# Optimization experiments

Hardware: AMD Instinct MI355X
Metric: run time of the kernel (lower is better)

## Reference

```python
import jax, jax.numpy as jnp
import numpy as np

B, F, H = 128, 12288, 2048   # batch, flattened-image dim (3x64x64), MLP hidden
TAU = 0.1                    # constraint(x) = relu(x@W1)@w2 - TAU  (so constraint(0) = -TAU < 0)
THRESHOLD = 1e-3
MAX_STEPS = 30


def setup_inputs() -> dict:
    key = jax.random.key(0)
    k1, k2, k3 = jax.random.split(key, 3)
    x0 = jnp.zeros((B, F), jnp.float32)                 # anchor point, constraint(x0) < 0 by construction
    x = jax.random.normal(k1, (B, F), jnp.float32)
    W1 = jax.random.normal(k2, (F, H), jnp.float32) / np.float32(np.sqrt(F))
    w2 = jax.random.normal(k3, (H,), jnp.float32) / np.float32(np.sqrt(H))
    return {"x0": x0, "x": x, "W1": W1, "w2": w2}


def reference(x0, x, W1, w2):
    def fvals(c):  # per-sample constraint value at interpolation coeff c: [B]
        xc = (1.0 - c)[:, None] * x0 + c[:, None] * x
        return jax.nn.relu(xc @ W1) @ w2 - TAU

    # f(0) = -TAU < 0 (asserted in original). Check f(1): samples already feasible skip search.
    f1 = fvals(jnp.ones((B,), jnp.float32))
    inside = f1 <= 0.0

    a = jnp.zeros((B,), jnp.float32)
    b = jnp.ones((B,), jnp.float32)
    c = jnp.ones((B,), jnp.float32)
    done = inside  # feasible samples keep c = 1 (projected == x)

    def step(carry, _):
        a, b, c, done = carry
        cm = (a + b) * 0.5
        v = fvals(cm)
        upd = ~done
        hit = upd & (v >= -THRESHOLD) & (v < 0.0)   # -threshold <= f(c) < 0 -> converged
        go_a = upd & (v < 0.0) & ~hit               # same sign as f(a): move a
        go_b = upd & (v >= 0.0)                     # opposite sign: move b
        a = jnp.where(go_a, cm, a)
        b = jnp.where(go_b, cm, b)
        c = jnp.where(upd, cm, c)                   # freeze c once done
        done = done | hit
        return (a, b, c, done), None

    (a, b, c, done), _ = jax.lax.scan(step, (a, b, c, done), None, length=MAX_STEPS)

    c = jnp.where(inside, 1.0, c)
    proj = (1.0 - c)[:, None] * x0 + c[:, None] * x
    # Original raises ConvergenceError -> NaN fill for non-converged samples.
    return jnp.where(done[:, None], proj, jnp.float32(jnp.nan))
```

## Files before the change

### kernel.cpp

```cpp
#include <hip/hip_runtime.h>
#include <hip/hip_bf16.h>

#define BB 128
#define FF 12288
#define HH 2048
#define TAU_F 0.1f
#define THR_F 1e-3f
#define NKG (FF / 8)
#define BH (BB * HH)
#define NFLAGS 192

typedef __attribute__((ext_vector_type(4))) float f32x4;
typedef __attribute__((ext_vector_type(8))) short s16x8;
typedef __attribute__((ext_vector_type(8))) unsigned short u16x8;

#define AS1 __attribute__((address_space(1)))
#define AS3 __attribute__((address_space(3)))

__device__ __forceinline__ void bsplit(float v, unsigned short& h, unsigned short& l) {
    unsigned int u  = __float_as_uint(v);
    unsigned int rh = (u + 0x7fffu + ((u >> 16) & 1u)) >> 16;
    float hf = __uint_as_float(rh << 16);
    float lf = v - hf;
    unsigned int ul = __float_as_uint(lf);
    unsigned int rl = (ul + 0x7fffu + ((ul >> 16) & 1u)) >> 16;
    h = (unsigned short)rh;
    l = (unsigned short)rl;
}

__device__ __forceinline__ bool read_nz(const int* __restrict__ flags) {
    const int lane = threadIdx.x & 63;
    int v = 0;
    if (lane < NFLAGS / 4) {
        const int4 q = ((const int4*)flags)[lane];
        v = q.x | q.y | q.z | q.w;
    }
    return __any(v != 0);
}

__global__ __launch_bounds__(256) void presplit_kernel(
    const float* __restrict__ x, const float* __restrict__ x0,
    unsigned short* __restrict__ Ah, unsigned short* __restrict__ Al,
    int* __restrict__ flags) {
    const int z = blockIdx.y;
    const float* __restrict__ X = z ? x0 : x;
    unsigned short* AH = Ah + (size_t)z * NKG * BB * 8;
    unsigned short* AL = Al + (size_t)z * NKG * BB * 8;
    const int t = threadIdx.x;
    const int w = t >> 6, lane = t & 63;
    const int kg = blockIdx.x * 8 + (t & 7);
    __shared__ int snz[4];
    int tnz = 0;
#pragma unroll
    for (int r = 0; r < 4; ++r) {
        const int m = (t >> 3) + r * 32;
        const float* src = X + (size_t)m * FF + kg * 8;
        u16x8 hv, lv;
#pragma unroll
        for (int j = 0; j < 8; ++j) {
            const float v = src[j];
            tnz |= (v != 0.f);
            unsigned short h, lo;
            bsplit(v, h, lo);
            hv[j] = h; lv[j] = lo;
        }
        const size_t o = ((size_t)kg * BB + m) * 8;
        *(u16x8*)(AH + o) = hv;
        *(u16x8*)(AL + o) = lv;
    }
    if (z == 1) {
        const int wnz = __any(tnz != 0) ? 1 : 0;
        if (lane == 0) snz[w] = wnz;
        __syncthreads();
        if (t == 0) flags[blockIdx.x] = snz[0] | snz[1] | snz[2] | snz[3];
    }
}

__global__ __launch_bounds__(256, 3) void mfma_gemm_kernel(
    const unsigned short* __restrict__ Ah, const unsigned short* __restrict__ Al,
    const float* __restrict__ W1, float* __restrict__ P,
    const int* __restrict__ flags, int SK, int KC, int NIT) {
    const int z = blockIdx.y;
    if (z == 1 && !read_nz(flags)) return;

    const int nwg = gridDim.x;
    const int bx  = blockIdx.x;
    const int wg  = (bx & 7) * (nwg >> 3) + (bx >> 3);
    const int ct  = wg & 31;
    const int kc  = wg >> 5;

    const int t   = threadIdx.x;
    const int w   = t >> 6;
    const int l   = t & 63;
    const int kgl = l >> 4;
    const int li  = l & 15;

    __shared__ unsigned short lds[2][12288];

    const size_t zoffA = (size_t)z * NKG * BB * 8;
    const unsigned short* APH = Ah + zoffA;
    const unsigned short* APL = Al + zoffA;

    f32x4 acc[2][4];
#pragma unroll
    for (int mt = 0; mt < 2; ++mt)
#pragma unroll
        for (int nt = 0; nt < 4; ++nt) acc[mt][nt] = (f32x4)0.f;

    const int kbase = kc * KC;
    const int bkg = t >> 6;
    const int bn  = t & 63;

    auto stageB_load = [&](int it, float* v) {
        const float* src = W1 + (size_t)(kbase + it * 32 + bkg * 8) * HH + ct * 64 + bn;
#pragma unroll
        for (int j = 0; j < 8; ++j) v[j] = src[(size_t)j * HH];
    };
    auto stageB_write = [&](int buf, const float* v) {
        u16x8 hv, lv;
#pragma unroll
        for (int j = 0; j < 8; ++j) {
            unsigned short h, lo;
            bsplit(v[j], h, lo);
            hv[j] = h; lv[j] = lo;
        }
        unsigned short* d = &lds[buf][(bkg * 64 + bn) * 8];
        *(u16x8*)(d + 8192)  = hv;
        *(u16x8*)(d + 10240) = lv;
    };
    auto stageA = [&](int it, int buf) {
        const int kg0 = (kbase + it * 32) >> 3;
#pragma unroll
        for (int s = 0; s < 4; ++s) {
            const int slot = w * 4 + s;
            const int isLo = slot >> 3;
            const int sl   = slot & 7;
            const int kgq  = sl >> 1;
            const int mh   = sl & 1;
            const unsigned short* src = (isLo ? APL : APH)
                + ((size_t)(kg0 + kgq) * BB + mh * 64 + l) * 8;
            unsigned short* dst = &lds[buf][isLo * 4096 + (kgq * 128 + mh * 64) * 8];
            __builtin_amdgcn_global_load_lds((const AS1 void*)src, (AS3 void*)dst, 16, 0, 0);
        }
    };
    auto compute = [&](int buf) {
        const unsigned short* L = lds[buf];
        s16x8 fah[2], fal[2], fbh[4], fbl[4];
#pragma unroll
        for (int mt = 0; mt < 2; ++mt) {
            const int mo = (kgl * 128 + w * 32 + mt * 16 + li) * 8;
            fah[mt] = *(const s16x8*)&L[mo];
            fal[mt] = *(const s16x8*)&L[4096 + mo];
        }
#pragma unroll
        for (int nt = 0; nt < 4; ++nt) {
            const int no = (kgl * 64 + nt * 16 + li) * 8;
            fbh[nt] = *(const s16x8*)&L[8192 + no];
            fbl[nt] = *(const s16x8*)&L[10240 + no];
        }
#pragma unroll
        for (int mt = 0; mt < 2; ++mt)
#pragma unroll
            for (int nt = 0; nt < 4; ++nt) {
                acc[mt][nt] = __builtin_amdgcn_mfma_f32_16x16x32_bf16(fah[mt], fbh[nt], acc[mt][nt], 0, 0, 0);
                acc[mt][nt] = __builtin_amdgcn_mfma_f32_16x16x32_bf16(fah[mt], fbl[nt], acc[mt][nt], 0, 0, 0);
                acc[mt][nt] = __builtin_amdgcn_mfma_f32_16x16x32_bf16(fal[mt], fbh[nt], acc[mt][nt], 0, 0, 0);
            }
    };

    float bv[8];
    stageB_load(0, bv);
    stageA(0, 0);
    stageB_write(0, bv);
    __syncthreads();

    for (int it = 0; it < NIT; ++it) {
        const int cur = it & 1;
        const bool more = (it + 1 < NIT);
        float bnx[8];
        if (more) { stageB_load(it + 1, bnx); stageA(it + 1, cur ^ 1); }
        compute(cur);
        if (more) stageB_write(cur ^ 1, bnx);
        __syncthreads();
    }

    float* dst = P + (size_t)(z * SK + kc) * BH;
    const int r0 = w * 32 + (l >> 4) * 4;
    const int c0 = ct * 64 + li;
#pragma unroll
    for (int mt = 0; mt < 2; ++mt)
#pragma unroll
        for (int nt = 0; nt < 4; ++nt)
#pragma unroll
            for (int r = 0; r < 4; ++r)
                dst[(size_t)(r0 + mt * 16 + r) * HH + c0 + nt * 16] = acc[mt][nt][r];
}

__global__ __launch_bounds__(256) void zflags_kernel(
    const float4* __restrict__ x0, int* __restrict__ flags) {
    const int t = threadIdx.x;
    const int w = t >> 6, lane = t & 63;
    __shared__ int snz[4];
    int tnz = 0;
    const int base = blockIdx.x * 2048 + t;
#pragma unroll
    for (int j = 0; j < 8; ++j) {
        float4 v = x0[base + 256 * j];
        tnz |= (v.x != 0.f) | (v.y != 0.f) | (v.z != 0.f) | (v.w != 0.f);
    }
    const int wnz = __any(tnz != 0) ? 1 : 0;
    if (lane == 0) snz[w] = wnz;
    __syncthreads();
    if (t == 0) flags[blockIdx.x] = snz[0] | snz[1] | snz[2] | snz[3];
}

__global__ __launch_bounds__(256) void legacy_gemm_kernel(
    const float* __restrict__ x, const float* __restrict__ x0,
    const float* __restrict__ W1, float* __restrict__ P,
    const int* __restrict__ flags) {
    const int ct = blockIdx.x, z = blockIdx.z, t = threadIdx.x;
    if (z == 1 && !read_nz(flags)) return;
    const int cg = t & 7, rg = t >> 3;
    const int r0 = rg * 4, cc = ct * 64 + cg * 8;
    float acc[4][8];
#pragma unroll
    for (int i = 0; i < 4; ++i)
#pragma unroll
        for (int n = 0; n < 8; ++n) acc[i][n] = 0.f;
    const float* __restrict__ X = z ? x0 : x;
    for (int k = 0; k < FF; k += 4) {
        float xr[4][4];
#pragma unroll
        for (int i = 0; i < 4; ++i) {
            float4 v = *(const float4*)(X + (size_t)(r0 + i) * FF + k);
            xr[i][0] = v.x; xr[i][1] = v.y; xr[i][2] = v.z; xr[i][3] = v.w;
        }
        float wr[4][8];
#pragma unroll
        for (int j = 0; j < 4; ++j) {
            float4 a = *(const float4*)(W1 + (size_t)(k + j) * HH + cc);
            float4 b = *(const float4*)(W1 + (size_t)(k + j) * HH + cc + 4);
            wr[j][0] = a.x; wr[j][1] = a.y; wr[j][2] = a.z; wr[j][3] = a.w;
            wr[j][4] = b.x; wr[j][5] = b.y; wr[j][6] = b.z; wr[j][7] = b.w;
        }
#pragma unroll
        for (int j = 0; j < 4; ++j)
#pragma unroll
            for (int i = 0; i < 4; ++i)
#pragma unroll
                for (int n = 0; n < 8; ++n)
                    acc[i][n] = fmaf(xr[i][j], wr[j][n], acc[i][n]);
    }
    float* Pp = P + (size_t)z * BH;
#pragma unroll
    for (int i = 0; i < 4; ++i) {
        float4 o0, o1;
        o0.x = acc[i][0]; o0.y = acc[i][1]; o0.z = acc[i][2]; o0.w = acc[i][3];
        o1.x = acc[i][4]; o1.y = acc[i][5]; o1.z = acc[i][6]; o1.w = acc[i][7];
        *(float4*)(Pp + (size_t)(r0 + i) * HH + cc) = o0;
        *(float4*)(Pp + (size_t)(r0 + i) * HH + cc + 4) = o1;
    }
}

__global__ __launch_bounds__(1024) void bisect_write_kernel(
    const float* __restrict__ P, const float* __restrict__ w2,
    const float* __restrict__ x, const float* __restrict__ x0,
    const int* __restrict__ flags, float* __restrict__ out, int SK) {
    const int b = blockIdx.x;
    const int t = threadIdx.x;
    const int w = t >> 6;
    const int lane = t & 63;
    __shared__ float red[16];
    const bool nz = read_nz(flags);

    const float2* P1 = (const float2*)(P + (size_t)b * HH) + t;
    float2 u1 = {0.f, 0.f};
    for (int kc = 0; kc < SK; ++kc) {
        const float2 v = P1[(size_t)kc * (BH / 2)];
        u1.x += v.x; u1.y += v.y;
    }
    const float2 wv = ((const float2*)w2)[t];

    auto blockReduce = [&](float v) -> float {
#pragma unroll
        for (int off = 32; off > 0; off >>= 1) v += __shfl_xor(v, off);
        if (lane == 0) red[w] = v;
        __syncthreads();
        float s = 0.f;
#pragma unroll
        for (int i = 0; i < 16; ++i) s += red[i];
        __syncthreads();
        return s;
    };

    float c = 1.f;
    bool done = false;
    if (!nz) {
        float p = fmaf(fmaxf(u1.x, 0.f), wv.x, fmaxf(u1.y, 0.f) * wv.y);
        const float S = blockReduce(p);
        const float f1 = S - TAU_F;
        const bool inside = (f1 <= 0.f);
        float a = 0.f, bh = 1.f;
        done = inside;
        for (int it = 0; it < 30; ++it) {
            const float cm = 0.5f * (a + bh);
            const float v = cm * S - TAU_F;
            const bool upd  = !done;
            const bool hit  = upd && (v >= -THR_F) && (v < 0.f);
            const bool go_a = upd && (v < 0.f) && !hit;
            const bool go_b = upd && (v >= 0.f);
            a  = go_a ? cm : a;
            bh = go_b ? cm : bh;
            c  = upd  ? cm : c;
            done = done || hit;
        }
        c = inside ? 1.f : c;
    } else {
        const float2* P0 = (const float2*)(P + (size_t)(SK * BH) + (size_t)b * HH) + t;
        float2 u0 = {0.f, 0.f};
        for (int kc = 0; kc < SK; ++kc) {
            const float2 v = P0[(size_t)kc * (BH / 2)];
            u0.x += v.x; u0.y += v.y;
        }
        const float2 dd = {u1.x - u0.x, u1.y - u0.y};
        auto feval = [&](float cc) -> float {
            float p = fmaf(fmaxf(fmaf(cc, dd.x, u0.x), 0.f), wv.x,
                           fmaxf(fmaf(cc, dd.y, u0.y), 0.f) * wv.y);
            return blockReduce(p) - TAU_F;
        };
        const float f1 = feval(1.f);
        const bool inside = (f1 <= 0.f);
        float a = 0.f, bh = 1.f;
        done = inside;
        for (int it = 0; it < 30; ++it) {
            const float cm = 0.5f * (a + bh);
            const float v = feval(cm);
            const bool upd  = !done;
            const bool hit  = upd && (v >= -THR_F) && (v < 0.f);
            const bool go_a = upd && (v < 0.f) && !hit;
            const bool go_b = upd && (v >= 0.f);
            a  = go_a ? cm : a;
            bh = go_b ? cm : bh;
            c  = upd  ? cm : c;
            done = done || hit;
        }
        c = inside ? 1.f : c;
    }

    const float nanv = __int_as_float(0x7fc00000);
    const float4* xr  = (const float4*)(x  + (size_t)b * FF);
    const float4* x0r = (const float4*)(x0 + (size_t)b * FF);
    float4* orow = (float4*)(out + (size_t)b * FF);
    if (!done) {
        float4 o; o.x = o.y = o.z = o.w = nanv;
#pragma unroll
        for (int k2 = 0; k2 < 3; ++k2) orow[t + 1024 * k2] = o;
    } else if (!nz) {
#pragma unroll
        for (int k2 = 0; k2 < 3; ++k2) {
            const int i = t + 1024 * k2;
            float4 xv = xr[i], o;
            o.x = c * xv.x; o.y = c * xv.y; o.z = c * xv.z; o.w = c * xv.w;
            orow[i] = o;
        }
    } else {
#pragma unroll
        for (int k2 = 0; k2 < 3; ++k2) {
            const int i = t + 1024 * k2;
            float4 xv = xr[i], zv = x0r[i], o;
            o.x = fmaf(c, xv.x - zv.x, zv.x);
            o.y = fmaf(c, xv.y - zv.y, zv.y);
            o.z = fmaf(c, xv.z - zv.z, zv.z);
            o.w = fmaf(c, xv.w - zv.w, zv.w);
            orow[i] = o;
        }
    }
}

extern "C" void kernel_launch(void* const* d_in, const int* in_sizes, int n_in,
                              void* d_out, int out_size, void* d_ws, size_t ws_size,
                              hipStream_t stream) {
    const float* x0 = (const float*)d_in[0];
    const float* x  = (const float*)d_in[1];
    const float* W1 = (const float*)d_in[2];
    const float* w2 = (const float*)d_in[3];
    float* out = (float*)d_out;
    char* ws = (char*)d_ws;

    const size_t szA   = (size_t)2 * NKG * BB * 8 * sizeof(unsigned short);
    const size_t offAl = szA;
    const size_t offFl = 2 * szA;
    const size_t offP  = offFl + 1024;

    int SK = 0;
    const int cand[5] = {16, 8, 4, 2, 1};
    for (int i = 0; i < 5; ++i) {
        const size_t need = offP + (size_t)2 * cand[i] * BH * sizeof(float);
        if (ws_size >= need) { SK = cand[i]; break; }
    }

    if (SK > 0) {
        unsigned short* Ah = (unsigned short*)ws;
        unsigned short* Al = (unsigned short*)(ws + offAl);
        int*   flags = (int*)(ws + offFl);
        float* P     = (float*)(ws + offP);
        const int KC = FF / SK, NIT = KC / 32;

        presplit_kernel<<<dim3(NKG / 8, 2), 256, 0, stream>>>(x, x0, Ah, Al, flags);
        mfma_gemm_kernel<<<dim3(32 * SK, 2), 256, 0, stream>>>(Ah, Al, W1, P, flags, SK, KC, NIT);
        bisect_write_kernel<<<BB, 1024, 0, stream>>>(P, w2, x, x0, flags, out, SK);
    } else {
        float* P     = (float*)ws;
        int*   flags = (int*)(ws + (size_t)2 * BH * sizeof(float));
        zflags_kernel<<<NFLAGS, 256, 0, stream>>>((const float4*)x0, flags);
        legacy_gemm_kernel<<<dim3(32, 1, 2), 256, 0, stream>>>(x, x0, W1, P, flags);
        bisect_write_kernel<<<BB, 1024, 0, stream>>>(P, w2, x, x0, flags, out, 1);
    }
}
```

Before: 50.13 us.

## Load A fragments directly to registers, shrink LDS, raise occupancy and split-K

The A operand (pre-split bf16 hi/lo activations) is now read straight from global memory into registers instead of being staged through LDS with global_load_lds, so LDS only holds the W1 tile and drops from 48KB to 16KB. The main loop is unrolled by two with explicit even/odd register sets for A, and the plain __syncthreads is replaced by a custom waitcnt-plus-barrier. Launch bounds go from 3 to 4 waves per EU and split-K candidates change from 16 to 24, which adds more workgroups and a larger partial-sum buffer for the bisection kernel to reduce. Per-lane uncoalesced A loads and more register pressure are the tradeoff; the barrier only waits on lgkmcnt, so it relies on the W1 global loads having been consumed into LDS writes before it.

```diff
diff --git a/kernel.cpp b/kernel.cpp
--- a/kernel.cpp
+++ b/kernel.cpp
@@ -14,8 +14,9 @@
 typedef __attribute__((ext_vector_type(8))) short s16x8;
 typedef __attribute__((ext_vector_type(8))) unsigned short u16x8;
 
-#define AS1 __attribute__((address_space(1)))
-#define AS3 __attribute__((address_space(3)))
+__device__ __forceinline__ void barrier_lds() {
+    asm volatile("s_waitcnt lgkmcnt(0)\ns_barrier" ::: "memory");
+}
 
 __device__ __forceinline__ void bsplit(float v, unsigned short& h, unsigned short& l) {
     unsigned int u  = __float_as_uint(v);
@@ -76,7 +77,7 @@
     }
 }
 
-__global__ __launch_bounds__(256, 3) void mfma_gemm_kernel(
+__global__ __launch_bounds__(256, 4) void mfma_gemm_kernel(
     const unsigned short* __restrict__ Ah, const unsigned short* __restrict__ Al,
     const float* __restrict__ W1, float* __restrict__ P,
     const int* __restrict__ flags, int SK, int KC, int NIT) {
@@ -95,7 +96,7 @@
     const int kgl = l >> 4;
     const int li  = l & 15;
 
-    __shared__ unsigned short lds[2][12288];
+    __shared__ unsigned short lds[2][4096];
 
     const size_t zoffA = (size_t)z * NKG * BB * 8;
     const unsigned short* APH = Ah + zoffA;
@@ -108,8 +109,20 @@
         for (int nt = 0; nt < 4; ++nt) acc[mt][nt] = (f32x4)0.f;
 
     const int kbase = kc * KC;
+    const int kg0   = kbase >> 3;
     const int bkg = t >> 6;
     const int bn  = t & 63;
+
+    s16x8 ahE[2], alE[2], ahO[2], alO[2];
+    auto loadA = [&](s16x8* ah, s16x8* al, int it) {
+        const int kg = kg0 + it * 4 + kgl;
+#pragma unroll
+        for (int mt = 0; mt < 2; ++mt) {
+            const size_t o = ((size_t)kg * BB + w * 32 + mt * 16 + li) * 8;
+            ah[mt] = *(const s16x8*)(APH + o);
+            al[mt] = *(const s16x8*)(APL + o);
+        }
+    };
 
     auto stageB_load = [&](int it, float* v) {
         const float* src = W1 + (size_t)(kbase + it * 32 + bkg * 8) * HH + ct * 64 + bn;
@@ -125,63 +138,44 @@
             hv[j] = h; lv[j] = lo;
         }
         unsigned short* d = &lds[buf][(bkg * 64 + bn) * 8];
-        *(u16x8*)(d + 8192)  = hv;
-        *(u16x8*)(d + 10240) = lv;
+        *(u16x8*)(d)        = hv;
+        *(u16x8*)(d + 2048) = lv;
     };
-    auto stageA = [&](int it, int buf) {
-        const int kg0 = (kbase + it * 32) >> 3;
-#pragma unroll
-        for (int s = 0; s < 4; ++s) {
-            const int slot = w * 4 + s;
-            const int isLo = slot >> 3;
-            const int sl   = slot & 7;
-            const int kgq  = sl >> 1;
-            const int mh   = sl & 1;
-            const unsigned short* src = (isLo ? APL : APH)
-                + ((size_t)(kg0 + kgq) * BB + mh * 64 + l) * 8;
-            unsigned short* dst = &lds[buf][isLo * 4096 + (kgq * 128 + mh * 64) * 8];
-            __builtin_amdgcn_global_load_lds((const AS1 void*)src, (AS3 void*)dst, 16, 0, 0);
-        }
-    };
-    auto compute = [&](int buf) {
+    auto computeR = [&](const s16x8* ah, const s16x8* al, int buf) {
         const unsigned short* L = lds[buf];
-        s16x8 fah[2], fal[2], fbh[4], fbl[4];
-#pragma unroll
-        for (int mt = 0; mt < 2; ++mt) {
-            const int mo = (kgl * 128 + w * 32 + mt * 16 + li) * 8;
-            fah[mt] = *(const s16x8*)&L[mo];
-            fal[mt] = *(const s16x8*)&L[4096 + mo];
-        }
 #pragma unroll
         for (int nt = 0; nt < 4; ++nt) {
             const int no = (kgl * 64 + nt * 16 + li) * 8;
-            fbh[nt] = *(const s16x8*)&L[8192 + no];
-            fbl[nt] = *(const s16x8*)&L[10240 + no];
-        }
-#pragma unroll
-        for (int mt = 0; mt < 2; ++mt)
-#pragma unroll
-            for (int nt = 0; nt < 4; ++nt) {
-                acc[mt][nt] = __builtin_amdgcn_mfma_f32_16x16x32_bf16(fah[mt], fbh[nt], acc[mt][nt], 0, 0, 0);
-                acc[mt][nt] = __builtin_amdgcn_mfma_f32_16x16x32_bf16(fah[mt], fbl[nt], acc[mt][nt], 0, 0, 0);
-                acc[mt][nt] = __builtin_amdgcn_mfma_f32_16x16x32_bf16(fal[mt], fbh[nt], acc[mt][nt], 0, 0, 0);
+            const s16x8 fbh = *(const s16x8*)&L[no];
+            const s16x8 fbl = *(const s16x8*)&L[2048 + no];
+#pragma unroll
+            for (int mt = 0; mt < 2; ++mt) {
+                acc[mt][nt] = __builtin_amdgcn_mfma_f32_16x16x32_bf16(ah[mt], fbh, acc[mt][nt], 0, 0, 0);
+                acc[mt][nt] = __builtin_amdgcn_mfma_f32_16x16x32_bf16(ah[mt], fbl, acc[mt][nt], 0, 0, 0);
+                acc[mt][nt] = __builtin_amdgcn_mfma_f32_16x16x32_bf16(al[mt], fbh, acc[mt][nt], 0, 0, 0);
             }
+        }
     };
 
     float bv[8];
+    loadA(ahE, alE, 0);
     stageB_load(0, bv);
-    stageA(0, 0);
     stageB_write(0, bv);
-    __syncthreads();
-
-    for (int it = 0; it < NIT; ++it) {
-        const int cur = it & 1;
-        const bool more = (it + 1 < NIT);
-        float bnx[8];
-        if (more) { stageB_load(it + 1, bnx); stageA(it + 1, cur ^ 1); }
-        compute(cur);
-        if (more) stageB_write(cur ^ 1, bnx);
-        __syncthreads();
+    barrier_lds();
+
+    for (int it = 0; it < NIT; it += 2) {
+        const bool m1 = (it + 1 < NIT);
+        const bool m2 = (it + 2 < NIT);
+        if (m1) { stageB_load(it + 1, bv); loadA(ahO, alO, it + 1); }
+        computeR(ahE, alE, 0);
+        if (m1) stageB_write(1, bv);
+        barrier_lds();
+        if (m1) {
+            if (m2) { stageB_load(it + 2, bv); loadA(ahE, alE, it + 2); }
+            computeR(ahO, alO, 1);
+            if (m2) stageB_write(0, bv);
+            barrier_lds();
+        }
     }
 
     float* dst = P + (size_t)(z * SK + kc) * BH;
@@ -393,7 +387,7 @@
     const size_t offP  = offFl + 1024;
 
     int SK = 0;
-    const int cand[5] = {16, 8, 4, 2, 1};
+    const int cand[5] = {24, 12, 6, 3, 1};
     for (int i = 0; i < 5; ++i) {
         const size_t need = offP + (size_t)2 * cand[i] * BH * sizeof(float);
         if (ws_size >= need) { SK = cand[i]; break; }
```

New measurement: 50.53 us. About the same (+0.8%).
